# Kernel tuning notes

Measured on AMD Instinct MI355X. Metric: run time of the kernel, lower is better.

## Reference

```python
import jax, jax.numpy as jnp
import numpy as np

N_NODES = 50000
N_EDGES = 800000
D = 128

def setup_inputs() -> dict:
    key = jax.random.key(0)
    k1, k2, k3, k4 = jax.random.split(key, 4)
    x = jax.random.normal(k1, (N_NODES, D), dtype=jnp.float32)
    edge_index = jax.random.randint(k2, (2, N_EDGES), 0, N_NODES, dtype=jnp.int64)
    # nn.Linear params: W is (out_dim, in_dim), b is (out_dim,)
    W = jax.random.normal(k3, (D, D), dtype=jnp.float32) * (1.0 / np.sqrt(D))
    b = jax.random.normal(k4, (D,), dtype=jnp.float32) * 0.01
    return {"x": x, "edge_index": edge_index, "W": W, "b": b}

def reference(x, edge_index, W, b):
    row, col = edge_index[0], edge_index[1]
    h = x @ W.T + b                      # (N, D) linear projection
    msgs = h[col]                        # gather by source col, (E, D)
    agg = jax.ops.segment_sum(msgs, row, num_segments=N_NODES)  # scatter-add by row
    return agg + h                       # residual
```

## Files before the change

### kernel.cpp

```cpp
#include <hip/hip_runtime.h>

#define NN 50000
#define NE 800000
#define DD 128
#define TILE_M 64
#define WPAD 136
#define CAP 64

#define NBG ((NN + TILE_M - 1) / TILE_M)
#define ECHUNK 2048
#define NCH ((NE + ECHUNK - 1) / ECHUNK)
#define NBS (NCH * 8)

typedef __attribute__((ext_vector_type(8))) short short8;
typedef __attribute__((ext_vector_type(4))) float f32x4;

__device__ __forceinline__ unsigned short f2bf(float f) {
    unsigned int u = __float_as_uint(f);
    u += 0x7fffu + ((u >> 16) & 1u);
    return (unsigned short)(u >> 16);
}

__global__ __launch_bounds__(256) void fused_gemm_scatter(
    const float* __restrict__ x, const float* __restrict__ W,
    const float* __restrict__ b, const int* __restrict__ ei,
    float* __restrict__ out, unsigned short* __restrict__ hbf,
    int* __restrict__ deg, int* __restrict__ slots)
{
    if (blockIdx.x >= NBG) {
        const int part  = blockIdx.x & 7;
        const int chunk = (blockIdx.x - NBG) >> 3;
        const int base  = chunk * ECHUNK;
#pragma unroll
        for (int i = 0; i < 8; ++i) {
            const int e = base + i * 256 + threadIdx.x;
            if (e < NE) {
                const int r = ei[e];
                if ((r & 7) == part) {
                    const int c = ei[NE + e];
                    const int p = atomicAdd(&deg[r], 1);
                    if (p < CAP) slots[r * CAP + p] = c;
                }
            }
        }
        return;
    }

    __shared__ unsigned short Wl[128 * WPAD];
    __shared__ unsigned short xl[TILE_M * WPAD];

    const int t = threadIdx.x;

    for (int i = t; i < 128 * 32; i += 256) {
        const int r = i >> 5, c4 = (i & 31) << 2;
        const float4 w4 = *(const float4*)(W + r * 128 + c4);
        unsigned short* dst = &Wl[r * WPAD + c4];
        dst[0] = f2bf(w4.x); dst[1] = f2bf(w4.y);
        dst[2] = f2bf(w4.z); dst[3] = f2bf(w4.w);
    }

    const int row0 = blockIdx.x * TILE_M;
#pragma unroll
    for (int i = 0; i < 8; ++i) {
        const int idx = i * 256 + t;
        const int r = idx >> 5, c4 = (idx & 31) << 2;
        int gr = row0 + r; if (gr > NN - 1) gr = NN - 1;
        const float4 v = *(const float4*)(x + (size_t)gr * 128 + c4);
        unsigned short* dst = &xl[r * WPAD + c4];
        dst[0] = f2bf(v.x); dst[1] = f2bf(v.y);
        dst[2] = f2bf(v.z); dst[3] = f2bf(v.w);
    }

    const int lane = t & 63;
    const int wave = t >> 6;
    const int m16  = lane & 15;
    const int quad = lane >> 4;

    float bias[8];
#pragma unroll
    for (int nt = 0; nt < 8; ++nt) bias[nt] = b[nt * 16 + m16];

    __syncthreads();

    const int am = wave * 16 + m16;
    short8 afrag[4];
#pragma unroll
    for (int kc = 0; kc < 4; ++kc)
        afrag[kc] = *(const short8*)&xl[am * WPAD + kc * 32 + quad * 8];

    f32x4 acc[8];
#pragma unroll
    for (int nt = 0; nt < 8; ++nt) acc[nt] = (f32x4){0.f, 0.f, 0.f, 0.f};

#pragma unroll
    for (int kc = 0; kc < 4; ++kc) {
#pragma unroll
        for (int nt = 0; nt < 8; ++nt) {
            const short8 bfrag =
                *(const short8*)&Wl[(nt * 16 + m16) * WPAD + kc * 32 + quad * 8];
            acc[nt] = __builtin_amdgcn_mfma_f32_16x16x32_bf16(
                afrag[kc], bfrag, acc[nt], 0, 0, 0);
        }
    }

    const int rbase = row0 + wave * 16 + quad * 4;
#pragma unroll
    for (int nt = 0; nt < 8; ++nt) {
#pragma unroll
        for (int r = 0; r < 4; ++r) {
            const int grow = rbase + r;
            if (grow < NN) {
                const float v = acc[nt][r] + bias[nt];
                out[(size_t)grow * 128 + nt * 16 + m16] = v;
                hbf[(size_t)grow * 128 + nt * 16 + m16] = f2bf(v);
            }
        }
    }
}

__global__ __launch_bounds__(256) void agg_kernel(
    const int* __restrict__ deg, const int* __restrict__ slots,
    const unsigned short* __restrict__ hbf, float* __restrict__ out)
{
    const int n = (blockIdx.x * 256 + threadIdx.x) >> 6;
    if (n >= NN) return;
    const int lane = threadIdx.x & 63;
    const int g = lane >> 4;
    const int s = lane & 15;

    const int dn_raw = deg[n];
    const int idx    = slots[n * CAP + lane];
    float4 r0, r1;
    if (g == 0) {
        r0 = *(const float4*)(out + (size_t)n * 128 + s * 8);
        r1 = *(const float4*)(out + (size_t)n * 128 + s * 8 + 4);
    }
    const int dn = min(dn_raw, CAP);

    float acc[8];
#pragma unroll
    for (int i = 0; i < 8; ++i) acc[i] = 0.f;

    for (int k = 0; k < dn; k += 16) {
        uint4 p[4];
#pragma unroll
        for (int bb = 0; bb < 4; ++bb) {
            const int e = k + bb * 4 + g;
            const int c = __shfl(idx, e, 64);
            p[bb] = (uint4){0u, 0u, 0u, 0u};
            if (e < dn)
                p[bb] = *(const uint4*)(hbf + (size_t)c * 128 + s * 8);
        }
#pragma unroll
        for (int bb = 0; bb < 4; ++bb) {
            acc[0] += __uint_as_float(p[bb].x << 16);
            acc[1] += __uint_as_float(p[bb].x & 0xffff0000u);
            acc[2] += __uint_as_float(p[bb].y << 16);
            acc[3] += __uint_as_float(p[bb].y & 0xffff0000u);
            acc[4] += __uint_as_float(p[bb].z << 16);
            acc[5] += __uint_as_float(p[bb].z & 0xffff0000u);
            acc[6] += __uint_as_float(p[bb].w << 16);
            acc[7] += __uint_as_float(p[bb].w & 0xffff0000u);
        }
    }

#pragma unroll
    for (int i = 0; i < 8; ++i) acc[i] += __shfl_xor(acc[i], 16, 64);
#pragma unroll
    for (int i = 0; i < 8; ++i) acc[i] += __shfl_xor(acc[i], 32, 64);

    if (g == 0) {
        r0.x += acc[0]; r0.y += acc[1]; r0.z += acc[2]; r0.w += acc[3];
        r1.x += acc[4]; r1.y += acc[5]; r1.z += acc[6]; r1.w += acc[7];
        *(float4*)(out + (size_t)n * 128 + s * 8)     = r0;
        *(float4*)(out + (size_t)n * 128 + s * 8 + 4) = r1;
    }
}

extern "C" void kernel_launch(void* const* d_in, const int* in_sizes, int n_in,
                              void* d_out, int out_size, void* d_ws, size_t ws_size,
                              hipStream_t stream)
{
    const float* x  = (const float*)d_in[0];
    const int*   ei = (const int*)d_in[1];
    const float* W  = (const float*)d_in[2];
    const float* b  = (const float*)d_in[3];
    float* out = (float*)d_out;

    unsigned short* hbf   = (unsigned short*)d_ws;
    int*            slots = (int*)(hbf + (size_t)NN * DD);
    int*            deg   = slots + (size_t)NN * CAP;

    hipMemsetAsync(deg, 0, NN * sizeof(int), stream);

    fused_gemm_scatter<<<NBG + NBS, 256, 0, stream>>>(x, W, b, ei, out, hbf, deg, slots);

    agg_kernel<<<(NN * 64 + 255) / 256, 256, 0, stream>>>(deg, slots, hbf, out);
}
```

Baseline: 164.1 us.

## Split aggregation into four column-quarter launches with 16 edges per step

The aggregation is split into four sequential launches, each covering a 32-column slice of the feature dimension. Each wave now handles 16 edges per iteration with 4 lanes per edge. The intent is to shrink the working set of gathered hbf rows per pass so it fits better in cache. The cost is re-reading deg, slots and out four times, paying four launch overheads, and losing the shuffle-based index broadcast and the 4-deep load batching.

```diff
diff --git a/kernel.cpp b/kernel.cpp
--- a/kernel.cpp
+++ b/kernel.cpp
@@ -118,62 +118,55 @@
     }
 }
 
-__global__ __launch_bounds__(256) void agg_kernel(
+__global__ __launch_bounds__(256) void agg_q_kernel(
     const int* __restrict__ deg, const int* __restrict__ slots,
-    const unsigned short* __restrict__ hbf, float* __restrict__ out)
+    const unsigned short* __restrict__ hbf, float* __restrict__ out,
+    const int q)
 {
     const int n = (blockIdx.x * 256 + threadIdx.x) >> 6;
     if (n >= NN) return;
     const int lane = threadIdx.x & 63;
-    const int g = lane >> 4;
-    const int s = lane & 15;
+    const int g = lane >> 2;
+    const int s = lane & 3;
+    const int colbase = q * 32 + s * 8;
 
-    const int dn_raw = deg[n];
-    const int idx    = slots[n * CAP + lane];
+    const int dn = min(deg[n], CAP);
     float4 r0, r1;
     if (g == 0) {
-        r0 = *(const float4*)(out + (size_t)n * 128 + s * 8);
-        r1 = *(const float4*)(out + (size_t)n * 128 + s * 8 + 4);
+        r0 = *(const float4*)(out + (size_t)n * 128 + colbase);
+        r1 = *(const float4*)(out + (size_t)n * 128 + colbase + 4);
     }
-    const int dn = min(dn_raw, CAP);
 
     float acc[8];
 #pragma unroll
     for (int i = 0; i < 8; ++i) acc[i] = 0.f;
 
     for (int k = 0; k < dn; k += 16) {
-        uint4 p[4];
-#pragma unroll
-        for (int bb = 0; bb < 4; ++bb) {
-            const int e = k + bb * 4 + g;
-            const int c = __shfl(idx, e, 64);
-            p[bb] = (uint4){0u, 0u, 0u, 0u};
-            if (e < dn)
-                p[bb] = *(const uint4*)(hbf + (size_t)c * 128 + s * 8);
-        }
-#pragma unroll
-        for (int bb = 0; bb < 4; ++bb) {
-            acc[0] += __uint_as_float(p[bb].x << 16);
-            acc[1] += __uint_as_float(p[bb].x & 0xffff0000u);
-            acc[2] += __uint_as_float(p[bb].y << 16);
-            acc[3] += __uint_as_float(p[bb].y & 0xffff0000u);
-            acc[4] += __uint_as_float(p[bb].z << 16);
-            acc[5] += __uint_as_float(p[bb].z & 0xffff0000u);
-            acc[6] += __uint_as_float(p[bb].w << 16);
-            acc[7] += __uint_as_float(p[bb].w & 0xffff0000u);
-        }
+        const int c = slots[n * CAP + k + g];
+        uint4 p = (uint4){0u, 0u, 0u, 0u};
+        if (k + g < dn)
+            p = *(const uint4*)(hbf + (size_t)c * 128 + colbase);
+        acc[0] += __uint_as_float(p.x << 16);
+        acc[1] += __uint_as_float(p.x & 0xffff0000u);
+        acc[2] += __uint_as_float(p.y << 16);
+        acc[3] += __uint_as_float(p.y & 0xffff0000u);
+        acc[4] += __uint_as_float(p.z << 16);
+        acc[5] += __uint_as_float(p.z & 0xffff0000u);
+        acc[6] += __uint_as_float(p.w << 16);
+        acc[7] += __uint_as_float(p.w & 0xffff0000u);
     }
 
 #pragma unroll
-    for (int i = 0; i < 8; ++i) acc[i] += __shfl_xor(acc[i], 16, 64);
+    for (int off = 4; off <= 32; off <<= 1) {
 #pragma unroll
-    for (int i = 0; i < 8; ++i) acc[i] += __shfl_xor(acc[i], 32, 64);
+        for (int i = 0; i < 8; ++i) acc[i] += __shfl_xor(acc[i], off, 64);
+    }
 
     if (g == 0) {
         r0.x += acc[0]; r0.y += acc[1]; r0.z += acc[2]; r0.w += acc[3];
         r1.x += acc[4]; r1.y += acc[5]; r1.z += acc[6]; r1.w += acc[7];
-        *(float4*)(out + (size_t)n * 128 + s * 8)     = r0;
-        *(float4*)(out + (size_t)n * 128 + s * 8 + 4) = r1;
+        *(float4*)(out + (size_t)n * 128 + colbase)     = r0;
+        *(float4*)(out + (size_t)n * 128 + colbase + 4) = r1;
     }
 }
 
@@ -195,5 +188,7 @@
 
     fused_gemm_scatter<<<NBG + NBS, 256, 0, stream>>>(x, W, b, ei, out, hbf, deg, slots);
 
-    agg_kernel<<<(NN * 64 + 255) / 256, 256, 0, stream>>>(deg, slots, hbf, out);
+    const int agg_blocks = (NN * 64 + 255) / 256;
+    for (int q = 0; q < 4; ++q)
+        agg_q_kernel<<<agg_blocks, 256, 0, stream>>>(deg, slots, hbf, out, q);
 }
```

After: 212.3 us. +29.4%, slower.

## Merge GEMM, edge placement and aggregation into one persistent cooperative kernel

Applied to the files above, without the earlier changes.

Replaces the two kernel launches with one cooperative persistent kernel of 512 blocks. Each block loops over GEMM tiles and edge-placement chunks, with odd and even blocks doing them in opposite order. A grid-wide sync then separates this from a grid-stride aggregation loop. This removes a kernel launch and loads W into shared memory once per block instead of once per tile, at the cost of a grid barrier, lower parallelism from persistent blocks, and an occupancy limit that comes from the shared memory size.

```diff
diff --git a/kernel.cpp b/kernel.cpp
--- a/kernel.cpp
+++ b/kernel.cpp
@@ -1,4 +1,7 @@
 #include <hip/hip_runtime.h>
+#include <hip/hip_cooperative_groups.h>
+
+namespace cg = cooperative_groups;
 
 #define NN 50000
 #define NE 800000
@@ -11,6 +14,7 @@
 #define ECHUNK 2048
 #define NCH ((NE + ECHUNK - 1) / ECHUNK)
 #define NBS (NCH * 8)
+#define GRID 512
 
 typedef __attribute__((ext_vector_type(8))) short short8;
 typedef __attribute__((ext_vector_type(4))) float f32x4;
@@ -21,15 +25,13 @@
     return (unsigned short)(u >> 16);
 }
 
-__global__ __launch_bounds__(256) void fused_gemm_scatter(
-    const float* __restrict__ x, const float* __restrict__ W,
-    const float* __restrict__ b, const int* __restrict__ ei,
-    float* __restrict__ out, unsigned short* __restrict__ hbf,
-    int* __restrict__ deg, int* __restrict__ slots)
-{
-    if (blockIdx.x >= NBG) {
-        const int part  = blockIdx.x & 7;
-        const int chunk = (blockIdx.x - NBG) >> 3;
+__device__ __forceinline__ void do_placement(
+    const int* __restrict__ ei, int* __restrict__ deg, int* __restrict__ slots,
+    int bid)
+{
+    for (int vb = bid; vb < NBS; vb += GRID) {
+        const int part  = vb & 7;
+        const int chunk = vb >> 3;
         const int base  = chunk * ECHUNK;
 #pragma unroll
         for (int i = 0; i < 8; ++i) {
@@ -43,12 +45,15 @@
                 }
             }
         }
-        return;
-    }
-
-    __shared__ unsigned short Wl[128 * WPAD];
-    __shared__ unsigned short xl[TILE_M * WPAD];
-
+    }
+}
+
+__device__ __forceinline__ void do_gemm(
+    const float* __restrict__ x, const float* __restrict__ W,
+    const float* __restrict__ b, float* __restrict__ out,
+    unsigned short* __restrict__ hbf,
+    unsigned short* Wl, unsigned short* xl, int bid)
+{
     const int t = threadIdx.x;
 
     for (int i = t; i < 128 * 32; i += 256) {
@@ -59,18 +64,6 @@
         dst[2] = f2bf(w4.z); dst[3] = f2bf(w4.w);
     }
 
-    const int row0 = blockIdx.x * TILE_M;
-#pragma unroll
-    for (int i = 0; i < 8; ++i) {
-        const int idx = i * 256 + t;
-        const int r = idx >> 5, c4 = (idx & 31) << 2;
-        int gr = row0 + r; if (gr > NN - 1) gr = NN - 1;
-        const float4 v = *(const float4*)(x + (size_t)gr * 128 + c4);
-        unsigned short* dst = &xl[r * WPAD + c4];
-        dst[0] = f2bf(v.x); dst[1] = f2bf(v.y);
-        dst[2] = f2bf(v.z); dst[3] = f2bf(v.w);
-    }
-
     const int lane = t & 63;
     const int wave = t >> 6;
     const int m16  = lane & 15;
@@ -82,98 +75,133 @@
 
     __syncthreads();
 
-    const int am = wave * 16 + m16;
-    short8 afrag[4];
-#pragma unroll
-    for (int kc = 0; kc < 4; ++kc)
-        afrag[kc] = *(const short8*)&xl[am * WPAD + kc * 32 + quad * 8];
-
-    f32x4 acc[8];
-#pragma unroll
-    for (int nt = 0; nt < 8; ++nt) acc[nt] = (f32x4){0.f, 0.f, 0.f, 0.f};
-
-#pragma unroll
-    for (int kc = 0; kc < 4; ++kc) {
+    for (int tile = bid; tile < NBG; tile += GRID) {
+        const int row0 = tile * TILE_M;
+#pragma unroll
+        for (int i = 0; i < 8; ++i) {
+            const int idx = i * 256 + t;
+            const int r = idx >> 5, c4 = (idx & 31) << 2;
+            int gr = row0 + r; if (gr > NN - 1) gr = NN - 1;
+            const float4 v = *(const float4*)(x + (size_t)gr * 128 + c4);
+            unsigned short* dst = &xl[r * WPAD + c4];
+            dst[0] = f2bf(v.x); dst[1] = f2bf(v.y);
+            dst[2] = f2bf(v.z); dst[3] = f2bf(v.w);
+        }
+        __syncthreads();
+
+        const int am = wave * 16 + m16;
+        short8 afrag[4];
+#pragma unroll
+        for (int kc = 0; kc < 4; ++kc)
+            afrag[kc] = *(const short8*)&xl[am * WPAD + kc * 32 + quad * 8];
+
+        f32x4 acc[8];
+#pragma unroll
+        for (int nt = 0; nt < 8; ++nt) acc[nt] = (f32x4){0.f, 0.f, 0.f, 0.f};
+
+#pragma unroll
+        for (int kc = 0; kc < 4; ++kc) {
+#pragma unroll
+            for (int nt = 0; nt < 8; ++nt) {
+                const short8 bfrag =
+                    *(const short8*)&Wl[(nt * 16 + m16) * WPAD + kc * 32 + quad * 8];
+                acc[nt] = __builtin_amdgcn_mfma_f32_16x16x32_bf16(
+                    afrag[kc], bfrag, acc[nt], 0, 0, 0);
+            }
+        }
+
+        const int rbase = row0 + wave * 16 + quad * 4;
 #pragma unroll
         for (int nt = 0; nt < 8; ++nt) {
-            const short8 bfrag =
-                *(const short8*)&Wl[(nt * 16 + m16) * WPAD + kc * 32 + quad * 8];
-            acc[nt] = __builtin_amdgcn_mfma_f32_16x16x32_bf16(
-                afrag[kc], bfrag, acc[nt], 0, 0, 0);
-        }
-    }
-
-    const int rbase = row0 + wave * 16 + quad * 4;
-#pragma unroll
-    for (int nt = 0; nt < 8; ++nt) {
-#pragma unroll
-        for (int r = 0; r < 4; ++r) {
-            const int grow = rbase + r;
-            if (grow < NN) {
-                const float v = acc[nt][r] + bias[nt];
-                out[(size_t)grow * 128 + nt * 16 + m16] = v;
-                hbf[(size_t)grow * 128 + nt * 16 + m16] = f2bf(v);
-            }
-        }
-    }
-}
-
-__global__ __launch_bounds__(256) void agg_kernel(
-    const int* __restrict__ deg, const int* __restrict__ slots,
-    const unsigned short* __restrict__ hbf, float* __restrict__ out)
-{
-    const int n = (blockIdx.x * 256 + threadIdx.x) >> 6;
-    if (n >= NN) return;
+#pragma unroll
+            for (int r = 0; r < 4; ++r) {
+                const int grow = rbase + r;
+                if (grow < NN) {
+                    const float v = acc[nt][r] + bias[nt];
+                    out[(size_t)grow * 128 + nt * 16 + m16] = v;
+                    hbf[(size_t)grow * 128 + nt * 16 + m16] = f2bf(v);
+                }
+            }
+        }
+        __syncthreads();
+    }
+}
+
+__global__ __launch_bounds__(256) void mega(
+    const float* __restrict__ x, const float* __restrict__ W,
+    const float* __restrict__ b, const int* __restrict__ ei,
+    float* __restrict__ out, unsigned short* __restrict__ hbf,
+    int* __restrict__ deg, int* __restrict__ slots)
+{
+    __shared__ unsigned short Wl[128 * WPAD];
+    __shared__ unsigned short xl[TILE_M * WPAD];
+
+    const int bid = blockIdx.x;
+
+    if (bid & 1) {
+        do_placement(ei, deg, slots, bid);
+        do_gemm(x, W, b, out, hbf, Wl, xl, bid);
+    } else {
+        do_gemm(x, W, b, out, hbf, Wl, xl, bid);
+        do_placement(ei, deg, slots, bid);
+    }
+
+    __threadfence();
+    cg::this_grid().sync();
+
     const int lane = threadIdx.x & 63;
+    const int wave = threadIdx.x >> 6;
     const int g = lane >> 4;
     const int s = lane & 15;
 
-    const int dn_raw = deg[n];
-    const int idx    = slots[n * CAP + lane];
-    float4 r0, r1;
-    if (g == 0) {
-        r0 = *(const float4*)(out + (size_t)n * 128 + s * 8);
-        r1 = *(const float4*)(out + (size_t)n * 128 + s * 8 + 4);
-    }
-    const int dn = min(dn_raw, CAP);
-
-    float acc[8];
-#pragma unroll
-    for (int i = 0; i < 8; ++i) acc[i] = 0.f;
-
-    for (int k = 0; k < dn; k += 16) {
-        uint4 p[4];
-#pragma unroll
-        for (int bb = 0; bb < 4; ++bb) {
-            const int e = k + bb * 4 + g;
-            const int c = __shfl(idx, e, 64);
-            p[bb] = (uint4){0u, 0u, 0u, 0u};
-            if (e < dn)
-                p[bb] = *(const uint4*)(hbf + (size_t)c * 128 + s * 8);
-        }
-#pragma unroll
-        for (int bb = 0; bb < 4; ++bb) {
-            acc[0] += __uint_as_float(p[bb].x << 16);
-            acc[1] += __uint_as_float(p[bb].x & 0xffff0000u);
-            acc[2] += __uint_as_float(p[bb].y << 16);
-            acc[3] += __uint_as_float(p[bb].y & 0xffff0000u);
-            acc[4] += __uint_as_float(p[bb].z << 16);
-            acc[5] += __uint_as_float(p[bb].z & 0xffff0000u);
-            acc[6] += __uint_as_float(p[bb].w << 16);
-            acc[7] += __uint_as_float(p[bb].w & 0xffff0000u);
-        }
-    }
-
-#pragma unroll
-    for (int i = 0; i < 8; ++i) acc[i] += __shfl_xor(acc[i], 16, 64);
-#pragma unroll
-    for (int i = 0; i < 8; ++i) acc[i] += __shfl_xor(acc[i], 32, 64);
-
-    if (g == 0) {
-        r0.x += acc[0]; r0.y += acc[1]; r0.z += acc[2]; r0.w += acc[3];
-        r1.x += acc[4]; r1.y += acc[5]; r1.z += acc[6]; r1.w += acc[7];
-        *(float4*)(out + (size_t)n * 128 + s * 8)     = r0;
-        *(float4*)(out + (size_t)n * 128 + s * 8 + 4) = r1;
+    for (int n = bid * 4 + wave; n < NN; n += GRID * 4) {
+        const int dn_raw = deg[n];
+        const int idx    = slots[n * CAP + lane];
+        float4 r0, r1;
+        if (g == 0) {
+            r0 = *(const float4*)(out + (size_t)n * 128 + s * 8);
+            r1 = *(const float4*)(out + (size_t)n * 128 + s * 8 + 4);
+        }
+        const int dn = min(dn_raw, CAP);
+
+        float acc[8];
+#pragma unroll
+        for (int i = 0; i < 8; ++i) acc[i] = 0.f;
+
+        for (int k = 0; k < dn; k += 16) {
+            uint4 p[4];
+#pragma unroll
+            for (int bb = 0; bb < 4; ++bb) {
+                const int e = k + bb * 4 + g;
+                const int c = __shfl(idx, e, 64);
+                p[bb] = (uint4){0u, 0u, 0u, 0u};
+                if (e < dn)
+                    p[bb] = *(const uint4*)(hbf + (size_t)c * 128 + s * 8);
+            }
+#pragma unroll
+            for (int bb = 0; bb < 4; ++bb) {
+                acc[0] += __uint_as_float(p[bb].x << 16);
+                acc[1] += __uint_as_float(p[bb].x & 0xffff0000u);
+                acc[2] += __uint_as_float(p[bb].y << 16);
+                acc[3] += __uint_as_float(p[bb].y & 0xffff0000u);
+                acc[4] += __uint_as_float(p[bb].z << 16);
+                acc[5] += __uint_as_float(p[bb].z & 0xffff0000u);
+                acc[6] += __uint_as_float(p[bb].w << 16);
+                acc[7] += __uint_as_float(p[bb].w & 0xffff0000u);
+            }
+        }
+
+#pragma unroll
+        for (int i = 0; i < 8; ++i) acc[i] += __shfl_xor(acc[i], 16, 64);
+#pragma unroll
+        for (int i = 0; i < 8; ++i) acc[i] += __shfl_xor(acc[i], 32, 64);
+
+        if (g == 0) {
+            r0.x += acc[0]; r0.y += acc[1]; r0.z += acc[2]; r0.w += acc[3];
+            r1.x += acc[4]; r1.y += acc[5]; r1.z += acc[6]; r1.w += acc[7];
+            *(float4*)(out + (size_t)n * 128 + s * 8)     = r0;
+            *(float4*)(out + (size_t)n * 128 + s * 8 + 4) = r1;
+        }
     }
 }
 
@@ -193,7 +221,7 @@
 
     hipMemsetAsync(deg, 0, NN * sizeof(int), stream);
 
-    fused_gemm_scatter<<<NBG + NBS, 256, 0, stream>>>(x, W, b, ei, out, hbf, deg, slots);
-
-    agg_kernel<<<(NN * 64 + 255) / 256, 256, 0, stream>>>(deg, slots, hbf, out);
-}
+    void* args[] = {(void*)&x, (void*)&W, (void*)&b, (void*)&ei,
+                    (void*)&out, (void*)&hbf, (void*)&deg, (void*)&slots};
+    hipLaunchCooperativeKernel((void*)mega, dim3(GRID), dim3(256), args, 0, stream);
+}
```

Result: slower. 324.1 us (+97.6%).
